# Kernel optimization log

Hardware: AMD Instinct MI355X
Metric: run time of the kernel (lower is better)

Reference implementation:

```python
import jax, jax.numpy as jnp
import numpy as np

ROPE_BASE = 100.0  # CroCo/InfiniteVGGT-style 2D RoPE base

def _rope_1d(sub, pos, base=ROPE_BASE):
    # sub: (B,H,N,half), pos: (B,N) float
    half = sub.shape[-1]
    quarter = half // 2
    inv_freq = 1.0 / (base ** (jnp.arange(quarter, dtype=jnp.float32) / quarter))
    ang = pos[:, None, :, None] * inv_freq  # (B,1,N,quarter)
    cos, sin = jnp.cos(ang), jnp.sin(ang)
    x1, x2 = sub[..., :quarter], sub[..., quarter:]
    return jnp.concatenate([x1 * cos - x2 * sin, x1 * sin + x2 * cos], axis=-1)

def rope_2d(t, positions):
    # t: (B,H,N,Dh); positions: (B,N,2) int (y,x)
    Dh = t.shape[-1]
    half = Dh // 2
    pos_f = positions.astype(t.dtype)
    y = _rope_1d(t[..., :half], pos_f[..., 0])
    x = _rope_1d(t[..., half:], pos_f[..., 1])
    return jnp.concatenate([y, x], axis=-1)

def setup_inputs() -> dict:
    key = jax.random.key(0)
    k1, k2, k3, k4 = jax.random.split(key, 4)
    B, N, C, H = 2, 2048, 1024, 16
    x = jax.random.normal(k1, (B, N, C), dtype=jnp.float32)
    positions = jax.random.randint(k2, (B, N, 2), 0, 64, dtype=jnp.int32)
    qkv_w = jax.random.normal(k3, (3 * C, C), dtype=jnp.float32) * (C ** -0.5)
    proj_w = jax.random.normal(k4, (C, C), dtype=jnp.float32) * (C ** -0.5)
    proj_b = jnp.zeros((C,), dtype=jnp.float32)
    return {"x": x, "positions": positions, "qkv_w": qkv_w, "proj_w": proj_w, "proj_b": proj_b}

def reference(x, positions, qkv_w, proj_w, proj_b):
    B, N, C = x.shape
    H = 16
    Dh = C // H
    scale = Dh ** -0.5
    qkv = (x @ qkv_w.T).reshape(B, N, 3, H, Dh).transpose(2, 0, 3, 1, 4)  # (3,B,H,N,Dh)
    q, k, v = qkv[0], qkv[1], qkv[2]
    q = rope_2d(q, positions)
    k = rope_2d(k, positions)
    attn = jnp.einsum('bhnd,bhmd->bhnm', q, k) * scale  # (B,H,N,N)
    attn = jax.nn.softmax(attn, axis=-1)
    out = jnp.einsum('bhnm,bhmd->bhnd', attn, v)  # (B,H,N,Dh)
    out = out.transpose(0, 2, 1, 3).reshape(B, N, C)
    return out @ proj_w.T + proj_b
```

## Files before the change

kernel.cpp:

```cpp
#include <hip/hip_runtime.h>
#include <cmath>

typedef unsigned short u16;
typedef unsigned int   u32;
typedef __attribute__((ext_vector_type(8))) __bf16 bf16x8;
typedef __attribute__((ext_vector_type(2))) __bf16 bf16x2;
typedef __attribute__((ext_vector_type(4))) float  f32x4;
typedef __attribute__((ext_vector_type(2))) unsigned int u32x2;

constexpr int BB = 2, SEQ = 2048, CH = 1024, NH = 16, DH = 64;

__device__ inline u16 f2bf(float f) {
    u32 u = __builtin_bit_cast(u32, f);
    u += 0x7FFF + ((u >> 16) & 1);
    return (u16)(u >> 16);
}
__device__ inline float bf2f(u16 b) { return __builtin_bit_cast(float, (u32)b << 16); }
__device__ inline u32 pkbf(float a, float b) {
#if __has_builtin(__builtin_amdgcn_cvt_pk_bf16_f32)
    bf16x2 r = __builtin_amdgcn_cvt_pk_bf16_f32(a, b);
    return __builtin_bit_cast(u32, r);
#else
    return (u32)f2bf(a) | ((u32)f2bf(b) << 16);
#endif
}
__device__ inline float fexp2(float x) {
#if __has_builtin(__builtin_amdgcn_exp2f)
    return __builtin_amdgcn_exp2f(x);
#else
    return exp2f(x);
#endif
}

__device__ inline void pl32swap(u32& a, u32& b) {
#if __has_builtin(__builtin_amdgcn_permlane32_swap)
    u32x2 r = __builtin_amdgcn_permlane32_swap(a, b, false, false);
    a = r.x; b = r.y;
#else
    const int ln = threadIdx.x & 63;
    u32 ax = (u32)__shfl_xor((int)a, 32), bx = (u32)__shfl_xor((int)b, 32);
    u32 na = (ln & 32) ? bx : a;
    u32 nb = (ln & 32) ? b : ax;
    a = na; b = nb;
#endif
}
__device__ inline void pl16swap(u32& a, u32& b) {
#if __has_builtin(__builtin_amdgcn_permlane16_swap)
    u32x2 r = __builtin_amdgcn_permlane16_swap(a, b, false, false);
    a = r.x; b = r.y;
#else
    const int ln = threadIdx.x & 63;
    u32 ax = (u32)__shfl_xor((int)a, 16), bx = (u32)__shfl_xor((int)b, 16);
    u32 na = (ln & 16) ? bx : a;
    u32 nb = (ln & 16) ? b : ax;
    a = na; b = nb;
#endif
}

__device__ inline void gld_lds16(const void* g, void* l) {
    __builtin_amdgcn_global_load_lds((const __attribute__((address_space(1))) void*)g,
                                     (__attribute__((address_space(3))) void*)l, 16, 0, 0);
}
__device__ inline f32x4 mfma16(bf16x8 a, bf16x8 b, f32x4 c) {
    return __builtin_amdgcn_mfma_f32_16x16x32_bf16(a, b, c, 0, 0, 0);
}
__device__ inline bf16x8 ld_frag(const u16* p) {
    return __builtin_bit_cast(bf16x8, *(const uint4*)p);
}

__global__ __launch_bounds__(256) void convert_kernel(const float* __restrict__ x,
                                                      const float* __restrict__ wq,
                                                      const float* __restrict__ wp,
                                                      u16* __restrict__ xb,
                                                      u16* __restrict__ wqb,
                                                      u16* __restrict__ wpb,
                                                      float2* __restrict__ tabq,
                                                      float2* __restrict__ tabk) {
    const int q = blockIdx.x * 256 + threadIdx.x;
    if (q >= 2097152) {
        const int idx = q - 2097152;
        if (idx < 1024) {
            const int p = idx >> 4, i = idx & 15;
            const float f = exp2f(-(float)i * 0.41524101186092f);
            float s, c;
            sincosf((float)p * f, &s, &c);
            tabk[idx] = make_float2(c, s);
            tabq[idx] = make_float2(c * 0.18033688011112042f,
                                    s * 0.18033688011112042f);
        }
        return;
    }
    const float* src; u16* dst; int idx;
    if (q < 1048576)            { src = x;  dst = xb;  idx = q; }
    else if (q < 1048576+786432){ src = wq; dst = wqb; idx = q - 1048576; }
    else                        { src = wp; dst = wpb; idx = q - 1048576 - 786432; }
    float4 v = *(const float4*)(src + (size_t)idx * 4);
    ushort4 o; o.x = f2bf(v.x); o.y = f2bf(v.y); o.z = f2bf(v.z); o.w = f2bf(v.w);
    *(ushort4*)(dst + (size_t)idx * 4) = o;
}

__global__ __launch_bounds__(256) void gemm_qkv_rope(const u16* __restrict__ A,
                                                     const u16* __restrict__ Bw,
                                                     const int* __restrict__ pos,
                                                     const float2* __restrict__ tabq,
                                                     const float2* __restrict__ tabk,
                                                     u16* __restrict__ Qb,
                                                     u16* __restrict__ Kb,
                                                     u16* __restrict__ Vt) {
    __shared__ u16 smem[18432];
    const int t = threadIdx.x, lane = t & 63, w = t >> 6;
    const int l15 = lane & 15, quad = lane >> 4;
    const int wm = w >> 1, wn = w & 1;
    const int m0 = blockIdx.y * 128, n0 = blockIdx.x * 128;
    const int K = CH;

    const int row0 = t >> 2, v0 = t & 3;
    const int gi0 = (v0 - (row0 >> 1)) & 3;
    const int row1 = row0 + 64;
    const int gi1 = (v0 - (row1 >> 1)) & 3;

    const u16* A0 = A  + (size_t)(m0 + row0) * K + gi0 * 8;
    const u16* A1 = A  + (size_t)(m0 + row1) * K + gi1 * 8;
    const u16* B0 = Bw + (size_t)(n0 + row0) * K + gi0 * 8;
    const u16* B1 = Bw + (size_t)(n0 + row1) * K + gi1 * 8;

    gld_lds16(A0, smem + t * 8);
    gld_lds16(A1, smem + 2048 + t * 8);
    gld_lds16(B0, smem + 8192 + t * 8);
    gld_lds16(B1, smem + 10240 + t * 8);

    f32x4 acc[4][4] = {};
    for (int kt = 0; kt < K / 32; ++kt) {
        __syncthreads();
        const int cur = (kt & 1) * 4096;
        if (kt + 1 < K / 32) {
            const int off = (kt + 1) * 32;
            const int nxt = ((kt + 1) & 1) * 4096;
            gld_lds16(A0 + off, smem + nxt + t * 8);
            gld_lds16(A1 + off, smem + nxt + 2048 + t * 8);
            gld_lds16(B0 + off, smem + 8192 + nxt + t * 8);
            gld_lds16(B1 + off, smem + 8192 + nxt + 2048 + t * 8);
        }
        const u16* as = smem + cur;
        const u16* bs = smem + 8192 + cur;
        bf16x8 af[4], bfv[4];
#pragma unroll
        for (int mi = 0; mi < 4; ++mi) {
            const int r = wm * 64 + mi * 16 + l15;
            af[mi] = ld_frag(as + (r * 4 + ((quad + (r >> 1)) & 3)) * 8);
        }
#pragma unroll
        for (int nj = 0; nj < 4; ++nj) {
            const int r = wn * 64 + nj * 16 + l15;
            bfv[nj] = ld_frag(bs + (r * 4 + ((quad + (r >> 1)) & 3)) * 8);
        }
#pragma unroll
        for (int mi = 0; mi < 4; ++mi)
#pragma unroll
            for (int nj = 0; nj < 4; ++nj)
                acc[mi][nj] = mfma16(af[mi], bfv[nj], acc[mi][nj]);
    }

    const int reg = n0 >> 10;
    const int h   = ((n0 & 1023) >> 6) + wn;
    __syncthreads();
    u16* T = smem + w * 4608;
    const int rsel = lane >> 3, csel = lane & 7;
    if (reg < 2) {
        const float2* tab = reg ? tabk : tabq;
        u16* dstb = reg ? Kb : Qb;
#pragma unroll
        for (int mi = 0; mi < 4; ++mi) {
#pragma unroll
            for (int r = 0; r < 4; ++r) {
                const int m = m0 + wm * 64 + mi * 16 + quad * 4 + r;
                const int2 pp = *(const int2*)(pos + m * 2);
                const float2 ty = tab[pp.x * 16 + l15];
                const float2 tx = tab[pp.y * 16 + l15];
                const float x1 = acc[mi][0][r], x2 = acc[mi][1][r];
                const float y1 = acc[mi][2][r], y2 = acc[mi][3][r];
                const int ml = (mi * 16 + quad * 4 + r) * 72;
                T[ml + l15]      = f2bf(x1 * ty.x - x2 * ty.y);
                T[ml + l15 + 16] = f2bf(x1 * ty.y + x2 * ty.x);
                T[ml + l15 + 32] = f2bf(y1 * tx.x - y2 * tx.y);
                T[ml + l15 + 48] = f2bf(y1 * tx.y + y2 * tx.x);
            }
        }
        const int mbase = m0 + wm * 64;
        const int bh = (mbase >> 11) * NH + h;
        const int nbase = mbase & 2047;
#pragma unroll
        for (int j = 0; j < 8; ++j) {
            const int row = rsel + j * 8;
            u16* gp = dstb + ((size_t)bh * SEQ + nbase + row) * 64 + csel * 8;
            *(uint4*)gp = *(const uint4*)&T[row * 72 + csel * 8];
        }
    } else {
#pragma unroll
        for (int mi = 0; mi < 4; ++mi)
#pragma unroll
            for (int nj = 0; nj < 4; ++nj)
#pragma unroll
                for (int r = 0; r < 4; ++r)
                    T[(nj * 16 + l15) * 72 + mi * 16 + quad * 4 + r] =
                        f2bf(acc[mi][nj][r]);
        const int bh = (m0 >> 11) * NH + h;
        const int nbase = (m0 & 2047) + wm * 64;
#pragma unroll
        for (int j = 0; j < 8; ++j) {
            const int d = rsel + j * 8;
            u16* gp = Vt + ((size_t)bh * 64 + d) * SEQ + nbase + csel * 8;
            *(uint4*)gp = *(const uint4*)&T[d * 72 + csel * 8];
        }
    }
}

__global__ __launch_bounds__(256, 8) void attn_mfma(const u16* __restrict__ Qb,
                                                    const u16* __restrict__ Kb,
                                                    const u16* __restrict__ Vt,
                                                    u16* __restrict__ Opart,
                                                    float* __restrict__ lpart) {
    __shared__ u16 Ks[4096];
    __shared__ u16 Vs[4096];
    const int t = threadIdx.x, lane = t & 63, w = t >> 6;
    const int l15 = lane & 15, quad = lane >> 4;

    const int id = blockIdx.x;
    const int c  = id & 7, r_ = id >> 3;
    const int j  = r_ >> 5, xq = r_ & 31;
    const int g  = c + 8 * j;
    const int bh = g & 31;
    const int z  = g >> 5;
    const int q0 = xq * 64;

    const int rowA = t >> 3, vA = t & 7;
    const int giA = (vA - rowA) & 7;
    const int rowB = rowA + 32;
    const int giB = (vA - rowB) & 7;

    const size_t kbase = (size_t)bh * SEQ * 64;
    const size_t vbase = (size_t)bh * 64 * SEQ;

    const uint4 ones_u = {0x3F803F80u, 0x3F803F80u, 0x3F803F80u, 0x3F803F80u};
    const bf16x8 onesf = __builtin_bit_cast(bf16x8, ones_u);

    bf16x8 aq[2];
#pragma unroll
    for (int ks = 0; ks < 2; ++ks)
        aq[ks] = ld_frag(Qb + ((size_t)bh * SEQ + q0 + w * 16 + l15) * 64
                         + ks * 32 + quad * 8);

#define STAGE(kt_)                                                                \
    {                                                                             \
        const int k0_ = z * 1024 + (kt_) * 64;                                    \
        gld_lds16(Kb + kbase + (size_t)(k0_ + rowA) * 64 + giA * 8,               \
                  &Ks[t * 8]);                                                    \
        gld_lds16(Kb + kbase + (size_t)(k0_ + rowB) * 64 + giB * 8,               \
                  &Ks[2048 + t * 8]);                                             \
        gld_lds16(Vt + vbase + (size_t)rowA * SEQ + k0_ + giA * 8,                \
                  &Vs[t * 8]);                                                    \
        gld_lds16(Vt + vbase + (size_t)rowB * SEQ + k0_ + giB * 8,                \
                  &Vs[2048 + t * 8]);                                             \
    }

    f32x4 oacc[4] = {};
    f32x4 lacc = {};

    for (int kt = 0; kt < 16; ++kt) {
        __syncthreads();
        STAGE(kt)
        __syncthreads();

        f32x4 sacc[4] = {};
        __builtin_amdgcn_s_setprio(1);
#pragma unroll
        for (int ks = 0; ks < 2; ++ks)
#pragma unroll
            for (int nk = 0; nk < 4; ++nk) {
                const int rK = nk * 16 + l15;
                const bf16x8 kf = ld_frag(Ks + (rK * 8 + (((ks * 4 + quad) + rK) & 7)) * 8);
                sacc[nk] = mfma16(kf, aq[ks], sacc[nk]);
            }
        __builtin_amdgcn_s_setprio(0);

        bf16x8 pa[2];
        {
            u32 W[4][2];
#pragma unroll
            for (int nk = 0; nk < 4; ++nk) {
                const float p0 = fexp2(sacc[nk][0]);
                const float p1 = fexp2(sacc[nk][1]);
                const float p2 = fexp2(sacc[nk][2]);
                const float p3 = fexp2(sacc[nk][3]);
                W[nk][0] = pkbf(p0, p1);
                W[nk][1] = pkbf(p2, p3);
            }
            u32 t0[4], t1[4];
            {
                u32 a = W[0][0], cc = W[1][0];
                pl32swap(a, cc); pl16swap(a, cc);
                t0[0] = a; t0[2] = cc;
            }
            {
                u32 a = W[0][1], cc = W[1][1];
                pl32swap(a, cc); pl16swap(a, cc);
                t0[1] = a; t0[3] = cc;
            }
            {
                u32 a = W[2][0], cc = W[3][0];
                pl32swap(a, cc); pl16swap(a, cc);
                t1[0] = a; t1[2] = cc;
            }
            {
                u32 a = W[2][1], cc = W[3][1];
                pl32swap(a, cc); pl16swap(a, cc);
                t1[1] = a; t1[3] = cc;
            }
            uint4 u0; u0.x = t0[0]; u0.y = t0[1]; u0.z = t0[2]; u0.w = t0[3];
            uint4 u1; u1.x = t1[0]; u1.y = t1[1]; u1.z = t1[2]; u1.w = t1[3];
            pa[0] = __builtin_bit_cast(bf16x8, u0);
            pa[1] = __builtin_bit_cast(bf16x8, u1);
        }

        __builtin_amdgcn_s_setprio(1);
        lacc = mfma16(pa[0], onesf, lacc);
        lacc = mfma16(pa[1], onesf, lacc);
#pragma unroll
        for (int ks = 0; ks < 2; ++ks)
#pragma unroll
            for (int nj = 0; nj < 4; ++nj) {
                const int rV = nj * 16 + l15;
                const bf16x8 vf = ld_frag(Vs + (rV * 8 + (((ks * 4 + quad) + rV) & 7)) * 8);
                oacc[nj] = mfma16(pa[ks], vf, oacc[nj]);
            }
        __builtin_amdgcn_s_setprio(0);
    }
#undef STAGE

    u16* ob = Opart + (size_t)z * 4194304;
#pragma unroll
    for (int r = 0; r < 4; ++r) {
        const int qrow = q0 + w * 16 + quad * 4 + r;
        if (l15 == 0)
            lpart[((size_t)z * 32 + bh) * SEQ + qrow] = lacc[r];
        const size_t orow = ((size_t)bh * SEQ + qrow) * 64;
#pragma unroll
        for (int nj = 0; nj < 4; ++nj)
            ob[orow + nj * 16 + l15] = f2bf(oacc[nj][r]);
    }
}

__global__ __launch_bounds__(256) void merge_kernel(const u16* __restrict__ Opart,
                                                    const float* __restrict__ lpart,
                                                    u16* __restrict__ Ob) {
    const int gid = blockIdx.x * 256 + threadIdx.x;
    const int d4 = gid & 15, q = (gid >> 4) & 2047, bh = gid >> 15;
    const size_t i1 = ((size_t)bh * SEQ + q) * 64 + d4 * 4;
    const size_t i2 = i1 + 4194304;
    const float inv = 1.0f / (lpart[(size_t)bh * SEQ + q] +
                              lpart[((size_t)32 + bh) * SEQ + q]);
    const ushort4 a = *(const ushort4*)(Opart + i1);
    const ushort4 b = *(const ushort4*)(Opart + i2);
    ushort4 o;
    o.x = f2bf((bf2f(a.x) + bf2f(b.x)) * inv);
    o.y = f2bf((bf2f(a.y) + bf2f(b.y)) * inv);
    o.z = f2bf((bf2f(a.z) + bf2f(b.z)) * inv);
    o.w = f2bf((bf2f(a.w) + bf2f(b.w)) * inv);
    const int b_ = bh >> 4, h = bh & 15;
    *(ushort4*)(Ob + ((size_t)(b_ * SEQ + q)) * CH + h * 64 + d4 * 4) = o;
}

__global__ __launch_bounds__(256) void gemm_proj(const u16* __restrict__ A,
                                                 const u16* __restrict__ Bw,
                                                 const float* __restrict__ bias,
                                                 float* __restrict__ C) {
    __shared__ u16 smem[12288];
    const int t = threadIdx.x, lane = t & 63, w = t >> 6;
    const int l15 = lane & 15, quad = lane >> 4;
    const int wm = w >> 1, wn = w & 1;
    const int m0 = blockIdx.y * 64, n0 = blockIdx.x * 128;
    const int K = CH, N = CH;

    const int row0 = t >> 2, v0 = t & 3;
    const int gi0 = (v0 - (row0 >> 1)) & 3;
    const int row1 = row0 + 64;
    const int gi1 = (v0 - (row1 >> 1)) & 3;

    const u16* A0 = A  + (size_t)(m0 + row0) * K + gi0 * 8;
    const u16* B0 = Bw + (size_t)(n0 + row0) * K + gi0 * 8;
    const u16* B1 = Bw + (size_t)(n0 + row1) * K + gi1 * 8;

    gld_lds16(A0, smem + t * 8);
    gld_lds16(B0, smem + 4096 + t * 8);
    gld_lds16(B1, smem + 4096 + 2048 + t * 8);

    f32x4 acc[2][4] = {};
    for (int kt = 0; kt < K / 32; ++kt) {
        __syncthreads();
        const int curA = (kt & 1) * 2048;
        const int curB = 4096 + (kt & 1) * 4096;
        if (kt + 1 < K / 32) {
            const int off = (kt + 1) * 32;
            const int nxtA = ((kt + 1) & 1) * 2048;
            const int nxtB = 4096 + ((kt + 1) & 1) * 4096;
            gld_lds16(A0 + off, smem + nxtA + t * 8);
            gld_lds16(B0 + off, smem + nxtB + t * 8);
            gld_lds16(B1 + off, smem + nxtB + 2048 + t * 8);
        }
        const u16* as = smem + curA;
        const u16* bs = smem + curB;
        bf16x8 af[2], bfv[4];
#pragma unroll
        for (int mi = 0; mi < 2; ++mi) {
            const int r = wm * 32 + mi * 16 + l15;
            af[mi] = ld_frag(as + (r * 4 + ((quad + (r >> 1)) & 3)) * 8);
        }
#pragma unroll
        for (int nj = 0; nj < 4; ++nj) {
            const int r = wn * 64 + nj * 16 + l15;
            bfv[nj] = ld_frag(bs + (r * 4 + ((quad + (r >> 1)) & 3)) * 8);
        }
#pragma unroll
        for (int mi = 0; mi < 2; ++mi)
#pragma unroll
            for (int nj = 0; nj < 4; ++nj)
                acc[mi][nj] = mfma16(af[mi], bfv[nj], acc[mi][nj]);
    }
#pragma unroll
    for (int mi = 0; mi < 2; ++mi)
#pragma unroll
        for (int nj = 0; nj < 4; ++nj) {
            const int n = n0 + wn * 64 + nj * 16 + l15;
            const float bv = bias[n];
#pragma unroll
            for (int r = 0; r < 4; ++r) {
                const int m = m0 + wm * 32 + mi * 16 + quad * 4 + r;
                C[(size_t)m * N + n] = acc[mi][nj][r] + bv;
            }
        }
}

extern "C" void kernel_launch(void* const* d_in, const int* in_sizes, int n_in,
                              void* d_out, int out_size, void* d_ws, size_t ws_size,
                              hipStream_t stream) {
    const float* x      = (const float*)d_in[0];
    const int*   pos    = (const int*)d_in[1];
    const float* qkv_w  = (const float*)d_in[2];
    const float* proj_w = (const float*)d_in[3];
    const float* proj_b = (const float*)d_in[4];
    float* out = (float*)d_out;

    u16* ws = (u16*)d_ws;
    u16* x_bf    = ws;
    u16* attn_bf = ws;
    u16* wq_bf   = ws + 4194304;
    float* lpart = (float*)(ws + 4194304);
    u16* wp_bf   = ws + 7340032;
    u16* Qb      = ws + 8388608;
    u16* Kb      = ws + 12582912;
    u16* Vt      = ws + 16777216;
    u16* Opart   = ws + 20971520;
    float2* tabq = (float2*)(ws + 20971520);
    float2* tabk = (float2*)(ws + 20971520 + 4096);

    const int M = BB * SEQ;

    convert_kernel<<<8196, 256, 0, stream>>>(x, qkv_w, proj_w, x_bf, wq_bf, wp_bf,
                                             tabq, tabk);
    gemm_qkv_rope<<<dim3(3 * CH / 128, M / 128), 256, 0, stream>>>(
        x_bf, wq_bf, pos, tabq, tabk, Qb, Kb, Vt);
    attn_mfma<<<2048, 256, 0, stream>>>(Qb, Kb, Vt, Opart, lpart);
    merge_kernel<<<4096, 256, 0, stream>>>(Opart, lpart, attn_bf);
    gemm_proj<<<dim3(CH / 128, M / 64), 256, 0, stream>>>(
        attn_bf, wp_bf, proj_b, out);
}
```

Measured before the change: 201.5 us.

## Drop split-key attention and merge kernel, double-buffer K/V staging in LDS

Each attention block now walks all 2048 keys for its head instead of half of them, so the separate merge kernel and the partial-output and partial-denominator buffers go away. Normalization by the row sum now happens in the attention epilogue, which writes bf16 straight into the [B,N,C] layout. K/V tiles are double-buffered in LDS: the next tile is prefetched while the current one is consumed, leaving one barrier per iteration. In exchange the grid halves to 1024 blocks, LDS per block doubles and the occupancy hint drops from 8 to 4, so there is less parallelism to hide latency.

```diff
diff --git a/kernel.cpp b/kernel.cpp
--- a/kernel.cpp
+++ b/kernel.cpp
@@ -215,22 +215,19 @@
     }
 }
 
-__global__ __launch_bounds__(256, 8) void attn_mfma(const u16* __restrict__ Qb,
+__global__ __launch_bounds__(256, 4) void attn_mfma(const u16* __restrict__ Qb,
                                                     const u16* __restrict__ Kb,
                                                     const u16* __restrict__ Vt,
-                                                    u16* __restrict__ Opart,
-                                                    float* __restrict__ lpart) {
-    __shared__ u16 Ks[4096];
-    __shared__ u16 Vs[4096];
+                                                    u16* __restrict__ Ob) {
+    __shared__ u16 Ks[2][4096];
+    __shared__ u16 Vs[2][4096];
     const int t = threadIdx.x, lane = t & 63, w = t >> 6;
     const int l15 = lane & 15, quad = lane >> 4;
 
     const int id = blockIdx.x;
     const int c  = id & 7, r_ = id >> 3;
     const int j  = r_ >> 5, xq = r_ & 31;
-    const int g  = c + 8 * j;
-    const int bh = g & 31;
-    const int z  = g >> 5;
+    const int bh = c + 8 * j;
     const int q0 = xq * 64;
 
     const int rowA = t >> 3, vA = t & 7;
@@ -250,26 +247,29 @@
         aq[ks] = ld_frag(Qb + ((size_t)bh * SEQ + q0 + w * 16 + l15) * 64
                          + ks * 32 + quad * 8);
 
-#define STAGE(kt_)                                                                \
+#define STAGE(kt_, buf_)                                                          \
     {                                                                             \
-        const int k0_ = z * 1024 + (kt_) * 64;                                    \
+        const int k0_ = (kt_) * 64;                                               \
         gld_lds16(Kb + kbase + (size_t)(k0_ + rowA) * 64 + giA * 8,               \
-                  &Ks[t * 8]);                                                    \
+                  &Ks[buf_][t * 8]);                                              \
         gld_lds16(Kb + kbase + (size_t)(k0_ + rowB) * 64 + giB * 8,               \
-                  &Ks[2048 + t * 8]);                                             \
+                  &Ks[buf_][2048 + t * 8]);                                       \
         gld_lds16(Vt + vbase + (size_t)rowA * SEQ + k0_ + giA * 8,                \
-                  &Vs[t * 8]);                                                    \
+                  &Vs[buf_][t * 8]);                                              \
         gld_lds16(Vt + vbase + (size_t)rowB * SEQ + k0_ + giB * 8,                \
-                  &Vs[2048 + t * 8]);                                             \
-    }
+                  &Vs[buf_][2048 + t * 8]);                                       \
+    }
+
+    STAGE(0, 0)
 
     f32x4 oacc[4] = {};
     f32x4 lacc = {};
 
-    for (int kt = 0; kt < 16; ++kt) {
+    for (int kt = 0; kt < 32; ++kt) {
         __syncthreads();
-        STAGE(kt)
-        __syncthreads();
+        if (kt + 1 < 32) STAGE(kt + 1, (kt + 1) & 1)
+        const u16* ksm = Ks[kt & 1];
+        const u16* vsm = Vs[kt & 1];
 
         f32x4 sacc[4] = {};
         __builtin_amdgcn_s_setprio(1);
@@ -278,7 +278,7 @@
 #pragma unroll
             for (int nk = 0; nk < 4; ++nk) {
                 const int rK = nk * 16 + l15;
-                const bf16x8 kf = ld_frag(Ks + (rK * 8 + (((ks * 4 + quad) + rK) & 7)) * 8);
+                const bf16x8 kf = ld_frag(ksm + (rK * 8 + (((ks * 4 + quad) + rK) & 7)) * 8);
                 sacc[nk] = mfma16(kf, aq[ks], sacc[nk]);
             }
         __builtin_amdgcn_s_setprio(0);
@@ -330,44 +330,23 @@
 #pragma unroll
             for (int nj = 0; nj < 4; ++nj) {
                 const int rV = nj * 16 + l15;
-                const bf16x8 vf = ld_frag(Vs + (rV * 8 + (((ks * 4 + quad) + rV) & 7)) * 8);
+                const bf16x8 vf = ld_frag(vsm + (rV * 8 + (((ks * 4 + quad) + rV) & 7)) * 8);
                 oacc[nj] = mfma16(pa[ks], vf, oacc[nj]);
             }
         __builtin_amdgcn_s_setprio(0);
     }
 #undef STAGE
 
-    u16* ob = Opart + (size_t)z * 4194304;
+    const int b_ = bh >> 4, h = bh & 15;
 #pragma unroll
     for (int r = 0; r < 4; ++r) {
         const int qrow = q0 + w * 16 + quad * 4 + r;
-        if (l15 == 0)
-            lpart[((size_t)z * 32 + bh) * SEQ + qrow] = lacc[r];
-        const size_t orow = ((size_t)bh * SEQ + qrow) * 64;
+        const float inv = 1.0f / lacc[r];
+        u16* gp = Ob + ((size_t)(b_ * SEQ + qrow)) * CH + h * 64;
 #pragma unroll
         for (int nj = 0; nj < 4; ++nj)
-            ob[orow + nj * 16 + l15] = f2bf(oacc[nj][r]);
-    }
-}
-
-__global__ __launch_bounds__(256) void merge_kernel(const u16* __restrict__ Opart,
-                                                    const float* __restrict__ lpart,
-                                                    u16* __restrict__ Ob) {
-    const int gid = blockIdx.x * 256 + threadIdx.x;
-    const int d4 = gid & 15, q = (gid >> 4) & 2047, bh = gid >> 15;
-    const size_t i1 = ((size_t)bh * SEQ + q) * 64 + d4 * 4;
-    const size_t i2 = i1 + 4194304;
-    const float inv = 1.0f / (lpart[(size_t)bh * SEQ + q] +
-                              lpart[((size_t)32 + bh) * SEQ + q]);
-    const ushort4 a = *(const ushort4*)(Opart + i1);
-    const ushort4 b = *(const ushort4*)(Opart + i2);
-    ushort4 o;
-    o.x = f2bf((bf2f(a.x) + bf2f(b.x)) * inv);
-    o.y = f2bf((bf2f(a.y) + bf2f(b.y)) * inv);
-    o.z = f2bf((bf2f(a.z) + bf2f(b.z)) * inv);
-    o.w = f2bf((bf2f(a.w) + bf2f(b.w)) * inv);
-    const int b_ = bh >> 4, h = bh & 15;
-    *(ushort4*)(Ob + ((size_t)(b_ * SEQ + q)) * CH + h * 64 + d4 * 4) = o;
+            gp[nj * 16 + l15] = f2bf(oacc[nj][r] * inv);
+    }
 }
 
 __global__ __launch_bounds__(256) void gemm_proj(const u16* __restrict__ A,
@@ -454,12 +433,10 @@
     u16* x_bf    = ws;
     u16* attn_bf = ws;
     u16* wq_bf   = ws + 4194304;
-    float* lpart = (float*)(ws + 4194304);
     u16* wp_bf   = ws + 7340032;
     u16* Qb      = ws + 8388608;
     u16* Kb      = ws + 12582912;
     u16* Vt      = ws + 16777216;
-    u16* Opart   = ws + 20971520;
     float2* tabq = (float2*)(ws + 20971520);
     float2* tabk = (float2*)(ws + 20971520 + 4096);
 
@@ -469,8 +446,7 @@
                                              tabq, tabk);
     gemm_qkv_rope<<<dim3(3 * CH / 128, M / 128), 256, 0, stream>>>(
         x_bf, wq_bf, pos, tabq, tabk, Qb, Kb, Vt);
-    attn_mfma<<<2048, 256, 0, stream>>>(Qb, Kb, Vt, Opart, lpart);
-    merge_kernel<<<4096, 256, 0, stream>>>(Opart, lpart, attn_bf);
+    attn_mfma<<<1024, 256, 0, stream>>>(Qb, Kb, Vt, attn_bf);
     gemm_proj<<<dim3(CH / 128, M / 64), 256, 0, stream>>>(
         attn_bf, wp_bf, proj_b, out);
 }
```

Result: faster. 197.4 us (-2.1%).
